# Kernel tuning notes

Hardware: AMD Instinct MI355X
Metric: run time of the kernel (lower is better)

Reference implementation:

```python
import math
import jax, jax.numpy as jnp
import numpy as np

HID_DIM = 1024
N_HEAD = 16
HEAD_DIM = HID_DIM // N_HEAD
NEG_FILL = -1e9


def _alibi_slopes(n_head: int) -> np.ndarray:
    """ALiBi per-head slopes (Press et al. 2021), matching get_slopes()."""
    main = 2 ** int(math.log2(n_head))
    m = (2.0 ** (-8.0 / main)) ** np.arange(1, 1 + main)
    if main < n_head:
        intra = (2.0 ** (-4.0 / main)) ** np.arange(1, 1 + 2 * (n_head - main), 2)
        m = np.concatenate([m, intra])
    return m.astype(np.float32)  # [H]


def setup_inputs() -> dict:
    key = jax.random.key(0)
    k1, k2, k3 = jax.random.split(key, 3)
    B, S = 2, 2048
    x = jax.random.normal(k1, (B, S, HID_DIM), dtype=jnp.float32)
    mask = jnp.ones((B, S), dtype=jnp.int32)
    Wqkv = jax.random.normal(k2, (HID_DIM, 3 * HID_DIM), dtype=jnp.float32) * 0.02
    Wout = jax.random.normal(k3, (HID_DIM, HID_DIM), dtype=jnp.float32) * 0.02
    return {"x": x, "mask": mask, "Wqkv": Wqkv, "Wout": Wout}


def reference(x, mask, Wqkv, Wout):
    B, S, _ = x.shape
    qkv = x @ Wqkv  # [B,S,3*hid]
    q, k, v = jnp.split(qkv, 3, axis=-1)
    k_cache, v_cache = k, v  # current_cache (pre-reshape, [B,S,hid])

    def to_heads(t):
        return t.reshape(B, S, N_HEAD, HEAD_DIM).transpose(0, 2, 1, 3)  # [B,H,S,Dh]

    q, k, v = to_heads(q), to_heads(k), to_heads(v)

    # NOTE: original code computes self.dk but never scales QK^T by it.
    scores = jnp.einsum('bhqd,bhkd->bhqk', q, k)  # [B,H,S,S]

    # ALiBi bias: tril(j - i), zero on/above diagonal elsewhere per torch.tril
    pos = jnp.arange(S)
    alibi = jnp.tril(pos[None, :] - pos[:, None]).astype(scores.dtype)  # [S,S]
    slopes = jnp.asarray(_alibi_slopes(N_HEAD))  # [H]
    scores = scores + slopes[None, :, None, None] * alibi[None, None]

    # padding mask broadcast over key dim: mask[:,None,None,:]
    scores = jnp.where(mask[:, None, None, :] == 0, NEG_FILL, scores)

    probs = jax.nn.softmax(scores, axis=-1)
    attn = jnp.einsum('bhqk,bhkd->bhqd', probs, v)  # [B,H,S,Dh]
    attn = attn.transpose(0, 2, 1, 3).reshape(B, S, HID_DIM)
    out = attn @ Wout  # dropout is identity in eval / p=0
    return out, k_cache, v_cache
```

## Files before the change

kernel.cpp:

```cpp
#include <hip/hip_runtime.h>
#include <cstdint>
#include <cstddef>

#define HID 1024
#define NH 16
#define DH 64
#define SEQ 2048
#define BATCH 2
#define BS (BATCH*SEQ)
#define LOG2E 1.4426950408889634f
#define PAD 68

typedef __attribute__((ext_vector_type(8))) short bf16x8;
typedef __attribute__((ext_vector_type(4))) float f32x4;

static __device__ __forceinline__ float fast_exp2(float x) {
    return __builtin_amdgcn_exp2f(x);
}

static __device__ __forceinline__ short f2bf(float f) {
    union { float f; unsigned u; } v; v.f = f;
    unsigned r = (v.u + 0x7FFFu + ((v.u >> 16) & 1u)) >> 16;
    return (short)r;
}
static __device__ __forceinline__ unsigned pack2(float a, float b) {
    return (unsigned)(unsigned short)f2bf(a) | ((unsigned)(unsigned short)f2bf(b) << 16);
}

__global__ __launch_bounds__(256)
void transpose_w(const float* __restrict__ Wqkv, const float* __restrict__ Wout,
                 short* __restrict__ wqkvT, short* __restrict__ woutT)
{
    __shared__ short tl[64][66];
    const int bid = blockIdx.x;
    const float* W; short* WT; int Nw, K, k0, n0;
    if (bid < 768) {
        W = Wqkv; WT = wqkvT; Nw = 3072; K = 1024;
        n0 = (bid % 48) * 64; k0 = (bid / 48) * 64;
    } else {
        W = Wout; WT = woutT; Nw = 1024; K = 1024;
        int b2 = bid - 768;
        n0 = (b2 & 15) * 64; k0 = (b2 >> 4) * 64;
    }
    const int t = threadIdx.x;
    const int r = t >> 2, c0 = (t & 3) * 16;
    const float* src = W + (size_t)(k0 + r) * Nw + n0 + c0;
    #pragma unroll
    for (int i = 0; i < 16; i += 4) {
        float4 f = *(const float4*)(src + i);
        tl[r][c0+i+0] = f2bf(f.x); tl[r][c0+i+1] = f2bf(f.y);
        tl[r][c0+i+2] = f2bf(f.z); tl[r][c0+i+3] = f2bf(f.w);
    }
    __syncthreads();
    short* dst = WT + (size_t)(n0 + r) * K + k0 + c0;
    unsigned buf[8];
    #pragma unroll
    for (int i = 0; i < 8; ++i) {
        unsigned lo = (unsigned short)tl[c0 + 2*i    ][r];
        unsigned hi = (unsigned short)tl[c0 + 2*i + 1][r];
        buf[i] = lo | (hi << 16);
    }
    *(uint4*)dst       = *(uint4*)&buf[0];
    *((uint4*)dst + 1) = *(uint4*)&buf[4];
}

template<int AMODE, int CMODE>
__global__ __launch_bounds__(256, 3)
void gemm_bf16(const void* __restrict__ Aptr, const short* __restrict__ Bt,
               float* __restrict__ Cf,
               float* __restrict__ kc, float* __restrict__ vc,
               short* __restrict__ qb, short* __restrict__ kb, short* __restrict__ vt,
               int M, int N, int K)
{
    __shared__ short As[128*72];
    __shared__ short Bs[128*72];
    const int t    = threadIdx.x;
    const int wave = t >> 6, lane = t & 63;
    const int quad = lane >> 4, l16 = lane & 15;
    const int wrow = (wave & 1) * 64, wcol = (wave >> 1) * 64;
    const int n0 = blockIdx.x * 128, m0 = blockIdx.y * 128;

    f32x4 acc[4][4];
    #pragma unroll
    for (int mi = 0; mi < 4; ++mi)
        #pragma unroll
        for (int nj = 0; nj < 4; ++nj) acc[mi][nj] = (f32x4){0.f,0.f,0.f,0.f};

    const int r  = t >> 1;
    const int c0 = (t & 1) * 32;

    for (int kt = 0; kt < K; kt += 64) {
        if (AMODE == 0) {
            const float* src = (const float*)Aptr + (size_t)(m0 + r) * K + kt + c0;
            #pragma unroll
            for (int i = 0; i < 4; ++i) {
                float4 f0 = *(const float4*)(src + i*8);
                float4 f1 = *(const float4*)(src + i*8 + 4);
                unsigned u[4] = {pack2(f0.x,f0.y), pack2(f0.z,f0.w),
                                 pack2(f1.x,f1.y), pack2(f1.z,f1.w)};
                *(uint4*)&As[r*72 + c0 + i*8] = *(uint4*)u;
            }
        } else {
            const short* src = (const short*)Aptr + (size_t)(m0 + r) * K + kt + c0;
            #pragma unroll
            for (int i = 0; i < 4; ++i)
                *(uint4*)&As[r*72 + c0 + i*8] = *(const uint4*)(src + i*8);
        }
        {
            const short* bsrc = Bt + (size_t)(n0 + r) * K + kt + c0;
            #pragma unroll
            for (int i = 0; i < 4; ++i)
                *(uint4*)&Bs[r*72 + c0 + i*8] = *(const uint4*)(bsrc + i*8);
        }
        __syncthreads();

        #pragma unroll
        for (int ks = 0; ks < 2; ++ks) {
            bf16x8 af[4], bfr[4];
            #pragma unroll
            for (int mi = 0; mi < 4; ++mi)
                af[mi] = *(const bf16x8*)&As[(wrow + mi*16 + l16)*72 + ks*32 + quad*8];
            #pragma unroll
            for (int nj = 0; nj < 4; ++nj)
                bfr[nj] = *(const bf16x8*)&Bs[(wcol + nj*16 + l16)*72 + ks*32 + quad*8];
            #pragma unroll
            for (int mi = 0; mi < 4; ++mi)
                #pragma unroll
                for (int nj = 0; nj < 4; ++nj)
                    acc[mi][nj] = __builtin_amdgcn_mfma_f32_16x16x32_bf16(
                        af[mi], bfr[nj], acc[mi][nj], 0, 0, 0);
        }
        __syncthreads();
    }

    const int region = (CMODE == 0) ? (n0 >> 10) : 0;
    #pragma unroll
    for (int mi = 0; mi < 4; ++mi) {
        int rbase = m0 + wrow + mi*16 + quad*4;
        #pragma unroll
        for (int nj = 0; nj < 4; ++nj) {
            int col = n0 + wcol + nj*16 + l16;
            if (CMODE == 1) {
                #pragma unroll
                for (int reg = 0; reg < 4; ++reg)
                    Cf[(size_t)(rbase + reg) * N + col] = acc[mi][nj][reg];
            } else {
                int c = col & 1023;
                if (region == 0) {
                    #pragma unroll
                    for (int reg = 0; reg < 4; ++reg)
                        qb[(size_t)(rbase + reg) * HID + c] = f2bf(acc[mi][nj][reg] * LOG2E);
                } else if (region == 1) {
                    #pragma unroll
                    for (int reg = 0; reg < 4; ++reg) {
                        float v = acc[mi][nj][reg];
                        kc[(size_t)(rbase + reg) * HID + c] = v;
                        if (kb) kb[(size_t)(rbase + reg) * HID + c] = f2bf(v);
                    }
                } else {
                    #pragma unroll
                    for (int reg = 0; reg < 4; ++reg)
                        vc[(size_t)(rbase + reg) * HID + c] = acc[mi][nj][reg];
                    if (vt) {
                        int b = rbase >> 11, s = rbase & 2047;
                        int h = c >> 6, d = c & 63;
                        unsigned u[2] = {pack2(acc[mi][nj][0], acc[mi][nj][1]),
                                         pack2(acc[mi][nj][2], acc[mi][nj][3])};
                        *(uint2*)&vt[((size_t)((b*16 + h)*64 + d)) * SEQ + s] = *(uint2*)u;
                    }
                }
            }
        }
    }
}

template<bool KVB>
__global__ __launch_bounds__(256, 4)
void attn_kernel(const short* qb,
                 const short* __restrict__ kb, const short* __restrict__ vtg,
                 const float* __restrict__ kc, const float* __restrict__ vc,
                 const int*   __restrict__ mask,
                 short* attn_b)
{
    __shared__ short Ks[64*PAD];
    __shared__ short Vs[64*PAD];
    __shared__ short Ps[64*PAD];
    __shared__ float Mk[64];

    const int t    = threadIdx.x;
    const int wave = t >> 6, lane = t & 63;
    const int quad = lane >> 4, l16 = lane & 15;

    const int blk = blockIdx.x;
    const int qt  = blk & 31;
    const int h   = (blk >> 5) & 15;
    const int b   = blk >> 9;
    const int q0  = qt * 64;
    const float slope2 = exp2f(-0.5f * (float)(h + 1)) * LOG2E;
    const int* mb = mask + b * SEQ;

    const int r  = t >> 2;
    const int c0 = (t & 3) * 16;

    bf16x8 aq[2];
    #pragma unroll
    for (int ks = 0; ks < 2; ++ks)
        aq[ks] = *(const bf16x8*)(qb + ((size_t)(b*SEQ + q0 + 16*wave + l16)) * HID
                                     + h*DH + ks*32 + quad*8);

    float ls[4];
    f32x4 Oacc[4];
    #pragma unroll
    for (int i = 0; i < 4; ++i) {
        ls[i] = 0.f;
        Oacc[i] = (f32x4){0.f,0.f,0.f,0.f};
    }

    if (KVB) {
        uint4 kr0, kr1, vr0, vr1; float mval = 0.f;
        const short* kbase = kb  + ((size_t)(b*SEQ + r)) * HID + h*DH + c0;
        const short* vbase = vtg + ((size_t)((b*NH + h)*DH + r)) * SEQ + c0;

        kr0 = *(const uint4*)(kbase);
        kr1 = *(const uint4*)(kbase + 8);
        vr0 = *(const uint4*)(vbase);
        vr1 = *(const uint4*)(vbase + 8);
        if (t < 64) mval = (mb[t] == 0) ? -2.0e9f : 0.f;

        for (int kt = 0; kt < 32; ++kt) {
            const int j0 = kt * 64;
            __syncthreads();

            *(uint4*)&Ks[r*PAD + c0]     = kr0;
            *(uint4*)&Ks[r*PAD + c0 + 8] = kr1;
            *(uint4*)&Vs[r*PAD + c0]     = vr0;
            *(uint4*)&Vs[r*PAD + c0 + 8] = vr1;
            if (t < 64) Mk[t] = mval;

            if (kt < 31) {
                const short* kn = kbase + (size_t)(j0 + 64) * HID;
                const short* vn = vbase + (j0 + 64);
                kr0 = *(const uint4*)(kn);
                kr1 = *(const uint4*)(kn + 8);
                vr0 = *(const uint4*)(vn);
                vr1 = *(const uint4*)(vn + 8);
                if (t < 64) mval = (mb[j0 + 64 + t] == 0) ? -2.0e9f : 0.f;
            }
            __syncthreads();

            f32x4 S[4];
            #pragma unroll
            for (int nt = 0; nt < 4; ++nt) S[nt] = (f32x4){0.f,0.f,0.f,0.f};
            #pragma unroll
            for (int ks = 0; ks < 2; ++ks) {
                bf16x8 bk[4];
                #pragma unroll
                for (int nt = 0; nt < 4; ++nt)
                    bk[nt] = *(const bf16x8*)&Ks[(nt*16 + l16)*PAD + ks*32 + quad*8];
                #pragma unroll
                for (int nt = 0; nt < 4; ++nt)
                    S[nt] = __builtin_amdgcn_mfma_f32_16x16x32_bf16(
                        aq[ks], bk[nt], S[nt], 0, 0, 0);
            }

            #pragma unroll
            for (int nt = 0; nt < 4; ++nt) {
                int j = j0 + nt*16 + l16;
                float mn = Mk[nt*16 + l16];
                float p[4];
                #pragma unroll
                for (int reg = 0; reg < 4; ++reg) {
                    int qi = q0 + 16*wave + quad*4 + reg;
                    int d  = j - qi; if (d > 0) d = 0;
                    p[reg] = fast_exp2(fmaf(slope2, (float)d, S[nt][reg]) + mn);
                    ls[reg] += p[reg];
                }
                #pragma unroll
                for (int reg = 0; reg < 4; ++reg)
                    Ps[(16*wave + quad*4 + reg)*PAD + nt*16 + l16] = f2bf(p[reg]);
            }

            #pragma unroll
            for (int ks = 0; ks < 2; ++ks) {
                bf16x8 ap = *(const bf16x8*)&Ps[(16*wave + l16)*PAD + ks*32 + quad*8];
                bf16x8 bv[4];
                #pragma unroll
                for (int nt = 0; nt < 4; ++nt)
                    bv[nt] = *(const bf16x8*)&Vs[(nt*16 + l16)*PAD + ks*32 + quad*8];
                #pragma unroll
                for (int nt = 0; nt < 4; ++nt)
                    Oacc[nt] = __builtin_amdgcn_mfma_f32_16x16x32_bf16(
                        ap, bv[nt], Oacc[nt], 0, 0, 0);
            }
        }
    } else {
        for (int kt = 0; kt < 32; ++kt) {
            const int j0 = kt * 64;
            __syncthreads();
            {
                const float* src = kc + ((size_t)(b*SEQ + j0 + r)) * HID + h*DH + c0;
                #pragma unroll
                for (int i = 0; i < 16; i += 4) {
                    float4 f = *(const float4*)(src + i);
                    *(unsigned*)&Ks[r*PAD + c0 + i]     = pack2(f.x, f.y);
                    *(unsigned*)&Ks[r*PAD + c0 + i + 2] = pack2(f.z, f.w);
                }
                int kp = t & 31, db = t >> 5;
                const float* v0 = vc + ((size_t)(b*SEQ + j0 + 2*kp)) * HID + h*DH + db*8;
                const float* v1 = v0 + HID;
                float4 a0 = *(const float4*)v0, a1 = *(const float4*)(v0 + 4);
                float4 b0 = *(const float4*)v1, b1 = *(const float4*)(v1 + 4);
                float va[8]  = {a0.x,a0.y,a0.z,a0.w,a1.x,a1.y,a1.z,a1.w};
                float vb2[8] = {b0.x,b0.y,b0.z,b0.w,b1.x,b1.y,b1.z,b1.w};
                #pragma unroll
                for (int i = 0; i < 8; ++i)
                    *(unsigned*)&Vs[(db*8 + i)*PAD + 2*kp] = pack2(va[i], vb2[i]);
                if (t < 64) Mk[t] = (mb[j0 + t] == 0) ? -2.0e9f : 0.f;
            }
            __syncthreads();

            f32x4 S[4];
            #pragma unroll
            for (int nt = 0; nt < 4; ++nt) S[nt] = (f32x4){0.f,0.f,0.f,0.f};
            #pragma unroll
            for (int ks = 0; ks < 2; ++ks) {
                bf16x8 bk[4];
                #pragma unroll
                for (int nt = 0; nt < 4; ++nt)
                    bk[nt] = *(const bf16x8*)&Ks[(nt*16 + l16)*PAD + ks*32 + quad*8];
                #pragma unroll
                for (int nt = 0; nt < 4; ++nt)
                    S[nt] = __builtin_amdgcn_mfma_f32_16x16x32_bf16(
                        aq[ks], bk[nt], S[nt], 0, 0, 0);
            }

            #pragma unroll
            for (int nt = 0; nt < 4; ++nt) {
                int j = j0 + nt*16 + l16;
                float mn = Mk[nt*16 + l16];
                float p[4];
                #pragma unroll
                for (int reg = 0; reg < 4; ++reg) {
                    int qi = q0 + 16*wave + quad*4 + reg;
                    int d  = j - qi; if (d > 0) d = 0;
                    p[reg] = fast_exp2(fmaf(slope2, (float)d, S[nt][reg]) + mn);
                    ls[reg] += p[reg];
                }
                #pragma unroll
                for (int reg = 0; reg < 4; ++reg)
                    Ps[(16*wave + quad*4 + reg)*PAD + nt*16 + l16] = f2bf(p[reg]);
            }

            #pragma unroll
            for (int ks = 0; ks < 2; ++ks) {
                bf16x8 ap = *(const bf16x8*)&Ps[(16*wave + l16)*PAD + ks*32 + quad*8];
                bf16x8 bv[4];
                #pragma unroll
                for (int nt = 0; nt < 4; ++nt)
                    bv[nt] = *(const bf16x8*)&Vs[(nt*16 + l16)*PAD + ks*32 + quad*8];
                #pragma unroll
                for (int nt = 0; nt < 4; ++nt)
                    Oacc[nt] = __builtin_amdgcn_mfma_f32_16x16x32_bf16(
                        ap, bv[nt], Oacc[nt], 0, 0, 0);
            }
        }
    }

    float rinv[4];
    #pragma unroll
    for (int reg = 0; reg < 4; ++reg) {
        float s0 = ls[reg];
        #pragma unroll
        for (int off = 1; off <= 8; off <<= 1) s0 += __shfl_xor(s0, off, 64);
        rinv[reg] = 1.0f / s0;
    }

    short* ap = attn_b + (size_t)b * SEQ * HID + h * DH;
    #pragma unroll
    for (int nt = 0; nt < 4; ++nt) {
        int dcol = nt*16 + l16;
        #pragma unroll
        for (int reg = 0; reg < 4; ++reg) {
            int row = q0 + 16*wave + quad*4 + reg;
            ap[(size_t)row * HID + dcol] = f2bf(Oacc[nt][reg] * rinv[reg]);
        }
    }
}

extern "C" void kernel_launch(void* const* d_in, const int* in_sizes, int n_in,
                              void* d_out, int out_size, void* d_ws, size_t ws_size,
                              hipStream_t stream)
{
    const float* x    = (const float*)d_in[0];
    const int*   mask = (const int*)  d_in[1];
    const float* Wqkv = (const float*)d_in[2];
    const float* Wout = (const float*)d_in[3];

    float* out = (float*)d_out;
    float* kc  = out + (size_t)BS * HID;
    float* vc  = kc  + (size_t)BS * HID;

    char*  ws    = (char*)d_ws;
    short* qb    = (short*)ws;
    short* wqkvT = (short*)(ws + (8u << 20));
    short* woutT = (short*)(ws + (14u << 20));
    const bool full = ws_size >= (32u << 20);
    short* kb = full ? (short*)(ws + (16u << 20)) : nullptr;
    short* vt = full ? (short*)(ws + (24u << 20)) : nullptr;

    transpose_w<<<dim3(1024), dim3(256), 0, stream>>>(Wqkv, Wout, wqkvT, woutT);

    gemm_bf16<0,0><<<dim3(24, 32), dim3(256), 0, stream>>>(
        x, wqkvT, nullptr, kc, vc, qb, kb, vt, BS, 3*HID, HID);

    if (full)
        attn_kernel<true><<<dim3(1024), dim3(256), 0, stream>>>(
            qb, kb, vt, kc, vc, mask, qb);
    else
        attn_kernel<false><<<dim3(1024), dim3(256), 0, stream>>>(
            qb, nullptr, nullptr, kc, vc, mask, qb);

    gemm_bf16<1,1><<<dim3(8, 32), dim3(256), 0, stream>>>(
        qb, woutT, out, nullptr, nullptr, nullptr, nullptr, nullptr, BS, HID, HID);
}
```

Measured before the change: 277.9 us.

## Pre-convert x to bf16 and stage GEMM tiles via direct global-to-LDS loads

The prep kernel now also converts x to bf16 into scratch space inside the output buffer, so the QKV GEMM reads bf16 A instead of converting fp32 in its load loop. Both GEMMs now fill their tiles with global_load_lds 16-byte direct-to-LDS loads instead of going through registers, and drop the padded LDS stride. The out-projection GEMM uses a 64-wide N tile, doubling its grid so more CUs are busy. The risks are extra memory traffic for the x conversion pass and LDS bank conflicts now that the row stride is an unpadded 64.

```diff
diff --git a/kernel.cpp b/kernel.cpp
--- a/kernel.cpp
+++ b/kernel.cpp
@@ -27,12 +27,34 @@
     return (unsigned)(unsigned short)f2bf(a) | ((unsigned)(unsigned short)f2bf(b) << 16);
 }
 
+typedef const __attribute__((address_space(1))) unsigned gas_u32;
+typedef __attribute__((address_space(3))) unsigned las_u32;
+static __device__ __forceinline__ void gload_lds16(const short* g, short* l) {
+    __builtin_amdgcn_global_load_lds((gas_u32*)g, (las_u32*)l, 16, 0, 0);
+}
+
 __global__ __launch_bounds__(256)
-void transpose_w(const float* __restrict__ Wqkv, const float* __restrict__ Wout,
-                 short* __restrict__ wqkvT, short* __restrict__ woutT)
+void prep(const float* __restrict__ Wqkv, const float* __restrict__ Wout,
+          const float* __restrict__ x,
+          short* __restrict__ wqkvT, short* __restrict__ woutT,
+          short* __restrict__ xb)
 {
     __shared__ short tl[64][66];
     const int bid = blockIdx.x;
+    const int t = threadIdx.x;
+
+    if (bid >= 1024) {
+        const float4* x4 = (const float4*)x;
+        uint2* xo = (uint2*)xb;
+        const int base = (bid - 1024) * 4096 + t;
+        #pragma unroll
+        for (int i = 0; i < 16; ++i) {
+            float4 f = x4[base + i*256];
+            xo[base + i*256] = make_uint2(pack2(f.x, f.y), pack2(f.z, f.w));
+        }
+        return;
+    }
+
     const float* W; short* WT; int Nw, K, k0, n0;
     if (bid < 768) {
         W = Wqkv; WT = wqkvT; Nw = 3072; K = 1024;
@@ -42,7 +64,6 @@
         int b2 = bid - 768;
         n0 = (b2 & 15) * 64; k0 = (b2 >> 4) * 64;
     }
-    const int t = threadIdx.x;
     const int r = t >> 2, c0 = (t & 3) * 16;
     const float* src = W + (size_t)(k0 + r) * Nw + n0 + c0;
     #pragma unroll
@@ -64,69 +85,59 @@
     *((uint4*)dst + 1) = *(uint4*)&buf[4];
 }
 
-template<int AMODE, int CMODE>
+template<int CMODE, int BN>
 __global__ __launch_bounds__(256, 3)
-void gemm_bf16(const void* __restrict__ Aptr, const short* __restrict__ Bt,
-               float* __restrict__ Cf,
-               float* __restrict__ kc, float* __restrict__ vc,
-               short* __restrict__ qb, short* __restrict__ kb, short* __restrict__ vt,
-               int M, int N, int K)
+void gemm_lds(const short* __restrict__ A, const short* __restrict__ Bt,
+              float* __restrict__ Cf,
+              float* __restrict__ kc, float* __restrict__ vc,
+              short* __restrict__ qb, short* __restrict__ kb, short* __restrict__ vt,
+              int M, int N, int K)
 {
-    __shared__ short As[128*72];
-    __shared__ short Bs[128*72];
+    constexpr int WN = BN / 2;
+    constexpr int NF = WN / 16;
+    __shared__ short As[128*64];
+    __shared__ short Bs[BN*64];
     const int t    = threadIdx.x;
     const int wave = t >> 6, lane = t & 63;
     const int quad = lane >> 4, l16 = lane & 15;
-    const int wrow = (wave & 1) * 64, wcol = (wave >> 1) * 64;
-    const int n0 = blockIdx.x * 128, m0 = blockIdx.y * 128;
-
-    f32x4 acc[4][4];
+    const int wrow = (wave & 1) * 64, wcol = (wave >> 1) * WN;
+    const int n0 = blockIdx.x * BN, m0 = blockIdx.y * 128;
+
+    f32x4 acc[4][NF];
     #pragma unroll
     for (int mi = 0; mi < 4; ++mi)
         #pragma unroll
-        for (int nj = 0; nj < 4; ++nj) acc[mi][nj] = (f32x4){0.f,0.f,0.f,0.f};
-
-    const int r  = t >> 1;
-    const int c0 = (t & 1) * 32;
+        for (int nj = 0; nj < NF; ++nj) acc[mi][nj] = (f32x4){0.f,0.f,0.f,0.f};
+
+    const int lr = lane >> 3;
+    const int lc = (lane & 7) * 8;
+    const short* Ab = A  + (size_t)(m0 + wave*32       + lr) * K + lc;
+    const short* Bb = Bt + (size_t)(n0 + wave*(BN/4)   + lr) * K + lc;
+    short* AsW = As + (wave*32)      * 64;
+    short* BsW = Bs + (wave*(BN/4))  * 64;
 
     for (int kt = 0; kt < K; kt += 64) {
-        if (AMODE == 0) {
-            const float* src = (const float*)Aptr + (size_t)(m0 + r) * K + kt + c0;
-            #pragma unroll
-            for (int i = 0; i < 4; ++i) {
-                float4 f0 = *(const float4*)(src + i*8);
-                float4 f1 = *(const float4*)(src + i*8 + 4);
-                unsigned u[4] = {pack2(f0.x,f0.y), pack2(f0.z,f0.w),
-                                 pack2(f1.x,f1.y), pack2(f1.z,f1.w)};
-                *(uint4*)&As[r*72 + c0 + i*8] = *(uint4*)u;
-            }
-        } else {
-            const short* src = (const short*)Aptr + (size_t)(m0 + r) * K + kt + c0;
-            #pragma unroll
-            for (int i = 0; i < 4; ++i)
-                *(uint4*)&As[r*72 + c0 + i*8] = *(const uint4*)(src + i*8);
-        }
-        {
-            const short* bsrc = Bt + (size_t)(n0 + r) * K + kt + c0;
-            #pragma unroll
-            for (int i = 0; i < 4; ++i)
-                *(uint4*)&Bs[r*72 + c0 + i*8] = *(const uint4*)(bsrc + i*8);
-        }
+        #pragma unroll
+        for (int i = 0; i < 4; ++i)
+            gload_lds16(Ab + (size_t)(i*8)*K + kt, AsW + i*512);
+        #pragma unroll
+        for (int i = 0; i < BN/32; ++i)
+            gload_lds16(Bb + (size_t)(i*8)*K + kt, BsW + i*512);
         __syncthreads();
 
         #pragma unroll
         for (int ks = 0; ks < 2; ++ks) {
-            bf16x8 af[4], bfr[4];
+            bf16x8 af[4], bfr[NF];
             #pragma unroll
             for (int mi = 0; mi < 4; ++mi)
-                af[mi] = *(const bf16x8*)&As[(wrow + mi*16 + l16)*72 + ks*32 + quad*8];
-            #pragma unroll
-            for (int nj = 0; nj < 4; ++nj)
-                bfr[nj] = *(const bf16x8*)&Bs[(wcol + nj*16 + l16)*72 + ks*32 + quad*8];
+                af[mi] = *(const bf16x8*)&As[(wrow + mi*16 + l16)*64 + ks*32 + quad*8];
+            #pragma unroll
+            for (int nj = 0; nj < NF; ++nj)
+                bfr[nj] = *(const bf16x8*)&Bs[(wcol + nj*16 + l16)*64 + ks*32 + quad*8];
             #pragma unroll
             for (int mi = 0; mi < 4; ++mi)
                 #pragma unroll
-                for (int nj = 0; nj < 4; ++nj)
+                for (int nj = 0; nj < NF; ++nj)
                     acc[mi][nj] = __builtin_amdgcn_mfma_f32_16x16x32_bf16(
                         af[mi], bfr[nj], acc[mi][nj], 0, 0, 0);
         }
@@ -138,7 +149,7 @@
     for (int mi = 0; mi < 4; ++mi) {
         int rbase = m0 + wrow + mi*16 + quad*4;
         #pragma unroll
-        for (int nj = 0; nj < 4; ++nj) {
+        for (int nj = 0; nj < NF; ++nj) {
             int col = n0 + wcol + nj*16 + l16;
             if (CMODE == 1) {
                 #pragma unroll
@@ -408,10 +419,12 @@
     short* kb = full ? (short*)(ws + (16u << 20)) : nullptr;
     short* vt = full ? (short*)(ws + (24u << 20)) : nullptr;
 
-    transpose_w<<<dim3(1024), dim3(256), 0, stream>>>(Wqkv, Wout, wqkvT, woutT);
-
-    gemm_bf16<0,0><<<dim3(24, 32), dim3(256), 0, stream>>>(
-        x, wqkvT, nullptr, kc, vc, qb, kb, vt, BS, 3*HID, HID);
+    short* xb = (short*)out;
+
+    prep<<<dim3(1280), dim3(256), 0, stream>>>(Wqkv, Wout, x, wqkvT, woutT, xb);
+
+    gemm_lds<0,128><<<dim3(24, 32), dim3(256), 0, stream>>>(
+        xb, wqkvT, nullptr, kc, vc, qb, kb, vt, BS, 3*HID, HID);
 
     if (full)
         attn_kernel<true><<<dim3(1024), dim3(256), 0, stream>>>(
@@ -420,6 +433,6 @@
         attn_kernel<false><<<dim3(1024), dim3(256), 0, stream>>>(
             qb, nullptr, nullptr, kc, vc, mask, qb);
 
-    gemm_bf16<1,1><<<dim3(8, 32), dim3(256), 0, stream>>>(
+    gemm_lds<1,64><<<dim3(16, 32), dim3(256), 0, stream>>>(
         qb, woutT, out, nullptr, nullptr, nullptr, nullptr, nullptr, BS, HID, HID);
 }
```

New measurement: 227.7 us. 1.22x faster.
